# Optimization experiments

Hardware: AMD Instinct MI355X
Metric: run time of the kernel (lower is better)

## Reference

```python
import jax, jax.numpy as jnp
import numpy as np

COMMITMENT_COST = 0.25
NUM_CODES = 4096
EMBED_DIM = 64


def setup_inputs() -> dict:
    key = jax.random.key(0)
    k1, k2 = jax.random.split(key)
    z_e = jax.random.normal(k1, (65536, EMBED_DIM), dtype=jnp.float32)
    embeddings = jax.random.normal(k2, (NUM_CODES, EMBED_DIM), dtype=jnp.float32)
    return {"z_e": z_e, "embeddings": embeddings}


def reference(z_e, embeddings):
    # Squared Euclidean distances; argmin is identical to torch.cdist argmin.
    # d2[n,k] = |z_e[n]|^2 - 2 z_e[n].e[k] + |e[k]|^2
    z_sq = jnp.sum(z_e * z_e, axis=-1, keepdims=True)            # [N,1]
    e_sq = jnp.sum(embeddings * embeddings, axis=-1)              # [K]
    d2 = z_sq - 2.0 * jnp.einsum('nd,kd->nk', z_e, embeddings) + e_sq  # [N,K]
    indices = jnp.argmin(d2, axis=-1)                             # [N] int
    z_q = embeddings[indices]                                     # [N,D] gather

    # commitment loss = mse(stop_grad(z_q), z_e)
    commitment_loss = COMMITMENT_COST * jnp.mean(
        (jax.lax.stop_gradient(z_q) - z_e) ** 2)

    # straight-through estimator
    z_q_st = z_e + jax.lax.stop_gradient(z_q - z_e)

    # code usage stats: one-hot mean == normalized histogram (scatter-add)
    n = z_e.shape[0]
    counts = jnp.zeros((NUM_CODES,), dtype=jnp.float32).at[indices].add(1.0)
    avg_probs = counts / n
    perplexity = jnp.exp(-jnp.sum(avg_probs * jnp.log(avg_probs + 1e-10)))
    n_active = jnp.sum(avg_probs > 0.001)

    return z_q_st, indices, commitment_loss, perplexity, n_active
```

## Files before the change

kernel.cpp:

```cpp
#include <hip/hip_runtime.h>
#include <math.h>

#define D 64
#define K 4096
#define MARGIN 0.08f
#define KSPLIT 4
#define CPH (K / 16 / KSPLIT)

typedef float f32x4 __attribute__((ext_vector_type(4)));
typedef _Float16 f16x8 __attribute__((ext_vector_type(8)));

__global__ __launch_bounds__(256) void esplit_kernel(const float* __restrict__ emb,
                                                     short* __restrict__ e_h,
                                                     float* __restrict__ e_sq,
                                                     int* __restrict__ counts) {
  int i = blockIdx.x * 256 + threadIdx.x;
  {
    int lane = i & 63;
    int t = (i >> 6) & 1;
    int c = i >> 7;
    int quad = lane >> 4, col = lane & 15;
    const float* src = emb + (size_t)(c * 16 + col) * D + t * 32 + quad * 8;
    f32x4 u0 = *(const f32x4*)src;
    f32x4 u1 = *(const f32x4*)(src + 4);
    f16x8 h;
#pragma unroll
    for (int j = 0; j < 8; ++j) {
      float x = (j < 4) ? u0[j] : u1[j - 4];
      h[j] = (_Float16)x;
    }
    *(f16x8*)(e_h + (size_t)i * 8) = h;
  }
  if (i < K) {
    counts[i] = 0;
    const float* e = emb + (size_t)i * D;
    float s = 0.f;
#pragma unroll
    for (int d = 0; d < D; ++d) s = fmaf(e[d], e[d], s);
    e_sq[i] = s;
  }
}

__global__ __launch_bounds__(256, 2) void dist_kernel(const float* __restrict__ z_e,
                                                      const short* __restrict__ e_h,
                                                      const float* __restrict__ esq,
                                                      float* __restrict__ pbest,
                                                      float* __restrict__ psec,
                                                      int* __restrict__ pidx) {
  const int tid = threadIdx.x;
  const int wv = tid >> 6;
  const int lane = tid & 63;
  const int quad = lane >> 4, col = lane & 15;
  const int rowbase = blockIdx.x * 128 + wv * 32;
  const int half = blockIdx.y;
  const int c0 = half * CPH;

  f16x8 a_hi[2][2], a_lo[2][2];
#pragma unroll
  for (int s = 0; s < 2; ++s) {
#pragma unroll
    for (int t = 0; t < 2; ++t) {
      const float* zr = z_e + (size_t)(rowbase + s * 16 + col) * D + t * 32 + quad * 8;
      f32x4 u0 = *(const f32x4*)zr;
      f32x4 u1 = *(const f32x4*)(zr + 4);
#pragma unroll
      for (int j = 0; j < 8; ++j) {
        float x = (j < 4) ? u0[j] : u1[j - 4];
        _Float16 h = (_Float16)x;
        a_hi[s][t][j] = h;
        a_lo[s][t][j] = (_Float16)(x - (float)h);
      }
    }
  }

  float best[8], second[8];
  int bidx[8];
#pragma unroll
  for (int i = 0; i < 8; ++i) {
    best[i] = -__builtin_inff();
    second[i] = -__builtin_inff();
    bidx[i] = 0;
  }

  const size_t lofs = (size_t)lane * 8;
  const short* pB = e_h + (size_t)c0 * 1024 + lofs;
  const float* pE = esq + c0 * 16 + col;
  f16x8 b0 = *(const f16x8*)pB;
  f16x8 b1 = *(const f16x8*)(pB + 512);
  float eq = *pE;

  for (int cc = 0; cc < CPH; ++cc) {
    pB += 1024;
    pE += 16;
    f16x8 n0 = *(const f16x8*)pB;
    f16x8 n1 = *(const f16x8*)(pB + 512);
    float neq = *pE;

    const float seed = -0.5f * eq;
    f32x4 acc0 = {seed, seed, seed, seed};
    f32x4 acc1 = {seed, seed, seed, seed};
    acc0 = __builtin_amdgcn_mfma_f32_16x16x32_f16(a_hi[0][0], b0, acc0, 0, 0, 0);
    acc1 = __builtin_amdgcn_mfma_f32_16x16x32_f16(a_hi[1][0], b0, acc1, 0, 0, 0);
    acc0 = __builtin_amdgcn_mfma_f32_16x16x32_f16(a_lo[0][0], b0, acc0, 0, 0, 0);
    acc1 = __builtin_amdgcn_mfma_f32_16x16x32_f16(a_lo[1][0], b0, acc1, 0, 0, 0);
    acc0 = __builtin_amdgcn_mfma_f32_16x16x32_f16(a_hi[0][1], b1, acc0, 0, 0, 0);
    acc1 = __builtin_amdgcn_mfma_f32_16x16x32_f16(a_hi[1][1], b1, acc1, 0, 0, 0);
    acc0 = __builtin_amdgcn_mfma_f32_16x16x32_f16(a_lo[0][1], b1, acc0, 0, 0, 0);
    acc1 = __builtin_amdgcn_mfma_f32_16x16x32_f16(a_lo[1][1], b1, acc1, 0, 0, 0);

#pragma unroll
    for (int r = 0; r < 4; ++r) {
      float a0 = acc0[r];
      float ob = best[r];
      best[r] = fmaxf(ob, a0);
      second[r] = __builtin_amdgcn_fmed3f(ob, a0, second[r]);
      bidx[r] = (a0 > ob) ? cc : bidx[r];
    }
#pragma unroll
    for (int r = 0; r < 4; ++r) {
      float a1 = acc1[r];
      float ob = best[4 + r];
      best[4 + r] = fmaxf(ob, a1);
      second[4 + r] = __builtin_amdgcn_fmed3f(ob, a1, second[4 + r]);
      bidx[4 + r] = (a1 > ob) ? cc : bidx[4 + r];
    }

    b0 = n0;
    b1 = n1;
    eq = neq;
  }

#pragma unroll
  for (int i = 0; i < 8; ++i) {
    float b = -2.f * best[i];
    float s2 = -2.f * second[i];
    int ix = (c0 + bidx[i]) * 16 + col;
#pragma unroll
    for (int off = 1; off < 16; off <<= 1) {
      float ob = __shfl_xor(b, off);
      float os = __shfl_xor(s2, off);
      int oi = __shfl_xor(ix, off);
      float ns = fminf(fminf(s2, os), fmaxf(b, ob));
      if (ob < b || (ob == b && oi < ix)) ix = oi;
      b = fminf(b, ob);
      s2 = ns;
    }
    if (col == 0) {
      int row = rowbase + (i >> 2) * 16 + quad * 4 + (i & 3);
      size_t o = (size_t)half * 65536 + row;
      pbest[o] = b;
      psec[o] = s2;
      pidx[o] = ix;
    }
  }
}

__global__ __launch_bounds__(256) void merge_resolve_kernel(const float* __restrict__ z_e,
                                                            const float* __restrict__ emb,
                                                            const float* __restrict__ esq,
                                                            const float* __restrict__ pbest,
                                                            const float* __restrict__ psec,
                                                            const int* __restrict__ pidx,
                                                            int* __restrict__ best_idx) {
  const int tid = threadIdx.x;
  __shared__ int wl[256];
  __shared__ int wn;
  __shared__ float zs[4][D];
  if (tid == 0) wn = 0;
  __syncthreads();

  {
    int row = blockIdx.x * 256 + tid;
    float b = pbest[row];
    float s2 = psec[row];
    int ix = pidx[row];
#pragma unroll
    for (int h = 1; h < KSPLIT; ++h) {
      size_t o = (size_t)h * 65536 + row;
      float bh = pbest[o];
      float sh = psec[o];
      int ih = pidx[o];
      s2 = fminf(fminf(s2, sh), fmaxf(b, bh));
      if (bh < b) ix = ih;
      b = fminf(b, bh);
    }
    best_idx[row] = ix;
    if (s2 - b < MARGIN) {
      int slot = atomicAdd(&wn, 1);
      wl[slot] = row;
    }
  }
  __syncthreads();

  const int n = wn;
  const int wave = tid >> 6;
  const int lane = tid & 63;

  for (int j = wave; j < n; j += 4) {
    const int row = wl[j];
    if (lane < 16) ((f32x4*)zs[wave])[lane] = *((const f32x4*)(z_e + (size_t)row * D) + lane);

    float pb[KSPLIT], ps[KSPLIT];
    int pi[KSPLIT];
    float B = __builtin_inff();
#pragma unroll
    for (int h = 0; h < KSPLIT; ++h) {
      size_t o = (size_t)h * 65536 + row;
      pb[h] = pbest[o];
      ps[h] = psec[o];
      pi[h] = pidx[o];
      B = fminf(B, pb[h]);
    }
    const float lim = B + MARGIN;

    float bv = __builtin_inff();
    int bi = 0;
#pragma unroll
    for (int h = 0; h < KSPLIT; ++h) {
      if (ps[h] < lim) {
        float hb = __builtin_inff();
        int hx = 0;
        for (int t = 0; t < 16; ++t) {
          int c = h * 1024 + t * 64 + lane;
          const f32x4* er = (const f32x4*)(emb + (size_t)c * D);
          f32x4 a = {0.f, 0.f, 0.f, 0.f};
#pragma unroll
          for (int i = 0; i < 16; ++i)
            a = __builtin_elementwise_fma(er[i], ((const f32x4*)zs[wave])[i], a);
          float dot = (a[0] + a[1]) + (a[2] + a[3]);
          float q = fmaf(-2.f, dot, esq[c]);
          if (q < hb) { hb = q; hx = c; }
        }
#pragma unroll
        for (int off = 32; off > 0; off >>= 1) {
          float ov = __shfl_down(hb, off);
          int oi = __shfl_down(hx, off);
          if (ov < hb || (ov == hb && oi < hx)) { hb = ov; hx = oi; }
        }
        hb = __shfl(hb, 0);
        hx = __shfl(hx, 0);
        if (hb < bv || (hb == bv && hx < bi)) { bv = hb; bi = hx; }
      } else if (pb[h] < lim) {
        int c = pi[h];
        float p = emb[(size_t)c * D + lane] * zs[wave][lane];
#pragma unroll
        for (int off = 1; off < 64; off <<= 1) p += __shfl_xor(p, off);
        float q = fmaf(-2.f, p, esq[c]);
        if (q < bv || (q == bv && c < bi)) { bv = q; bi = c; }
      }
    }
    if (lane == 0) best_idx[row] = bi;
  }
}

__global__ __launch_bounds__(256) void finalize_kernel(const float* __restrict__ z_e,
                                                       const float* __restrict__ emb,
                                                       const int* __restrict__ best_idx,
                                                       float* __restrict__ out_zq,
                                                       float* __restrict__ out_idx,
                                                       int* __restrict__ counts,
                                                       float* __restrict__ block_loss) {
  const int tid = threadIdx.x;
  const int wave = tid >> 6;
  const int lane = tid & 63;
  const int row = blockIdx.x * 4 + wave;

  int bidx = best_idx[row];
  float ze = z_e[(size_t)row * D + lane];
  float zq = emb[(size_t)bidx * D + lane];
  float st = ze + (zq - ze);
  out_zq[(size_t)row * D + lane] = st;

  float diff = zq - ze;
  float sq = diff * diff;
#pragma unroll
  for (int off = 32; off > 0; off >>= 1) sq += __shfl_down(sq, off);

  __shared__ float ls[4];
  if (lane == 0) {
    ls[wave] = sq;
    out_idx[row] = (float)bidx;
    atomicAdd(&counts[bidx], 1);
  }
  __syncthreads();
  if (tid == 0) block_loss[blockIdx.x] = ls[0] + ls[1] + ls[2] + ls[3];
}

__global__ __launch_bounds__(1024) void stats_kernel(const float* __restrict__ block_loss,
                                                     int nblocks,
                                                     const int* __restrict__ counts,
                                                     float* __restrict__ out_scalars,
                                                     int N) {
  const int tid = threadIdx.x;
  const int wave = tid >> 6;
  const int lane = tid & 63;

  float lsum = 0.f;
  for (int i = tid; i < nblocks; i += 1024) lsum += block_loss[i];

  float ent = 0.f;
  int act = 0;
  const float invN = 1.0f / (float)N;
  for (int k = tid; k < K; k += 1024) {
    float p = (float)counts[k] * invN;
    ent += p * logf(p + 1e-10f);
    act += (p > 0.001f) ? 1 : 0;
  }

#pragma unroll
  for (int off = 32; off > 0; off >>= 1) {
    lsum += __shfl_down(lsum, off);
    ent += __shfl_down(ent, off);
    act += __shfl_down(act, off);
  }

  __shared__ float sl[16], se[16];
  __shared__ int sa[16];
  if (lane == 0) { sl[wave] = lsum; se[wave] = ent; sa[wave] = act; }
  __syncthreads();
  if (tid == 0) {
    float L = 0.f, E = 0.f;
    int A = 0;
#pragma unroll
    for (int w = 0; w < 16; ++w) { L += sl[w]; E += se[w]; A += sa[w]; }
    out_scalars[0] = 0.25f * L / ((float)N * (float)D);
    out_scalars[1] = expf(-E);
    out_scalars[2] = (float)A;
  }
}

extern "C" void kernel_launch(void* const* d_in, const int* in_sizes, int n_in,
                              void* d_out, int out_size, void* d_ws, size_t ws_size,
                              hipStream_t stream) {
  const float* z_e = (const float*)d_in[0];
  const float* emb = (const float*)d_in[1];
  const int N = in_sizes[0] / D;

  float* out = (float*)d_out;
  float* out_zq = out;
  float* out_idx = out + (size_t)N * D;
  float* out_scalars = out + (size_t)N * (D + 1);

  char* ws = (char*)d_ws;
  size_t o = 0;
  int* counts = (int*)(ws + o);      o += 16384;
  o += 256;
  float* esq = (float*)(ws + o);     o += 16384;
  short* e_h = (short*)(ws + o);     o += (size_t)K * D * 2;
  o += 8192;
  float* pbest = (float*)(ws + o);   o += (size_t)KSPLIT * N * 4;
  float* psec = (float*)(ws + o);    o += (size_t)KSPLIT * N * 4;
  int* pidx = (int*)(ws + o);        o += (size_t)KSPLIT * N * 4;
  int* best_idx = (int*)(ws + o);    o += (size_t)N * 4;
  float* block_loss = (float*)(ws + o);

  esplit_kernel<<<(K / 16) * 2 * 64 / 256, 256, 0, stream>>>(emb, e_h, esq, counts);
  dist_kernel<<<dim3(N / 128, KSPLIT), 256, 0, stream>>>(z_e, e_h, esq,
                                                         pbest, psec, pidx);
  merge_resolve_kernel<<<N / 256, 256, 0, stream>>>(z_e, emb, esq, pbest, psec,
                                                    pidx, best_idx);
  finalize_kernel<<<N / 4, 256, 0, stream>>>(z_e, emb, best_idx, out_zq, out_idx,
                                             counts, block_loss);
  stats_kernel<<<1, 1024, 0, stream>>>(block_loss, N / 4, counts, out_scalars, N);
}
```

Baseline: 224.9 us.

## Fuse merge, finalize and stats into one tail kernel; unroll distance loop

Merges the merge/resolve, finalize and stats kernels into a single tail kernel. It keeps the per-row best indices in shared memory, accumulates the loss into 64 atomic slots, and uses a last-block-done counter so the final block computes the scalar statistics. This removes two kernel launches and the global round trips for best_idx and block_loss. Separately, the dist_kernel main loop is unrolled by two with register ping-pong for the prefetched B fragments, which removes the register copies. The fused kernel processes 128 rows per block and relies on threadfence and atomics for cross-block completion, so that single final block becomes a serial tail.

```diff
diff --git a/kernel.cpp b/kernel.cpp
--- a/kernel.cpp
+++ b/kernel.cpp
@@ -13,7 +13,8 @@
 __global__ __launch_bounds__(256) void esplit_kernel(const float* __restrict__ emb,
                                                      short* __restrict__ e_h,
                                                      float* __restrict__ e_sq,
-                                                     int* __restrict__ counts) {
+                                                     int* __restrict__ counts,
+                                                     int* __restrict__ ctrl) {
   int i = blockIdx.x * 256 + threadIdx.x;
   {
     int lane = i & 63;
@@ -31,6 +32,7 @@
     }
     *(f16x8*)(e_h + (size_t)i * 8) = h;
   }
+  if (i < 128) ctrl[i] = 0;
   if (i < K) {
     counts[i] = 0;
     const float* e = emb + (size_t)i * D;
@@ -40,6 +42,45 @@
     e_sq[i] = s;
   }
 }
+
+#define MFMA16(A, B, C) __builtin_amdgcn_mfma_f32_16x16x32_f16(A, B, C, 0, 0, 0)
+
+#define STEP(C0, C1, CEQ, N0, N1, NEQ, CC)                                   \
+  {                                                                          \
+    N0 = *(const f16x8*)(pB);                                                \
+    N1 = *(const f16x8*)(pB + 512);                                          \
+    NEQ = *pE;                                                               \
+    pB += 1024;                                                              \
+    pE += 16;                                                                \
+    const float seed = -0.5f * (CEQ);                                        \
+    f32x4 acc0 = {seed, seed, seed, seed};                                   \
+    f32x4 acc1 = {seed, seed, seed, seed};                                   \
+    acc0 = MFMA16(a_hi[0][0], C0, acc0);                                     \
+    acc1 = MFMA16(a_hi[1][0], C0, acc1);                                     \
+    acc0 = MFMA16(a_lo[0][0], C0, acc0);                                     \
+    acc1 = MFMA16(a_lo[1][0], C0, acc1);                                     \
+    acc0 = MFMA16(a_hi[0][1], C1, acc0);                                     \
+    acc1 = MFMA16(a_hi[1][1], C1, acc1);                                     \
+    acc0 = MFMA16(a_lo[0][1], C1, acc0);                                     \
+    acc1 = MFMA16(a_lo[1][1], C1, acc1);                                     \
+    const int cc_ = (CC);                                                    \
+    _Pragma("unroll")                                                        \
+    for (int r = 0; r < 4; ++r) {                                            \
+      float a0 = acc0[r];                                                    \
+      float ob = best[r];                                                    \
+      best[r] = fmaxf(ob, a0);                                               \
+      second[r] = __builtin_amdgcn_fmed3f(ob, a0, second[r]);                \
+      bidx[r] = (a0 > ob) ? cc_ : bidx[r];                                   \
+    }                                                                        \
+    _Pragma("unroll")                                                        \
+    for (int r = 0; r < 4; ++r) {                                            \
+      float a1 = acc1[r];                                                    \
+      float ob = best[4 + r];                                                \
+      best[4 + r] = fmaxf(ob, a1);                                           \
+      second[4 + r] = __builtin_amdgcn_fmed3f(ob, a1, second[4 + r]);        \
+      bidx[4 + r] = (a1 > ob) ? cc_ : bidx[4 + r];                           \
+    }                                                                        \
+  }
 
 __global__ __launch_bounds__(256, 2) void dist_kernel(const float* __restrict__ z_e,
                                                       const short* __restrict__ e_h,
@@ -82,52 +123,19 @@
     bidx[i] = 0;
   }
 
-  const size_t lofs = (size_t)lane * 8;
-  const short* pB = e_h + (size_t)c0 * 1024 + lofs;
+  const short* pB = e_h + (size_t)c0 * 1024 + (size_t)lane * 8;
   const float* pE = esq + c0 * 16 + col;
   f16x8 b0 = *(const f16x8*)pB;
   f16x8 b1 = *(const f16x8*)(pB + 512);
   float eq = *pE;
-
-  for (int cc = 0; cc < CPH; ++cc) {
-    pB += 1024;
-    pE += 16;
-    f16x8 n0 = *(const f16x8*)pB;
-    f16x8 n1 = *(const f16x8*)(pB + 512);
-    float neq = *pE;
-
-    const float seed = -0.5f * eq;
-    f32x4 acc0 = {seed, seed, seed, seed};
-    f32x4 acc1 = {seed, seed, seed, seed};
-    acc0 = __builtin_amdgcn_mfma_f32_16x16x32_f16(a_hi[0][0], b0, acc0, 0, 0, 0);
-    acc1 = __builtin_amdgcn_mfma_f32_16x16x32_f16(a_hi[1][0], b0, acc1, 0, 0, 0);
-    acc0 = __builtin_amdgcn_mfma_f32_16x16x32_f16(a_lo[0][0], b0, acc0, 0, 0, 0);
-    acc1 = __builtin_amdgcn_mfma_f32_16x16x32_f16(a_lo[1][0], b0, acc1, 0, 0, 0);
-    acc0 = __builtin_amdgcn_mfma_f32_16x16x32_f16(a_hi[0][1], b1, acc0, 0, 0, 0);
-    acc1 = __builtin_amdgcn_mfma_f32_16x16x32_f16(a_hi[1][1], b1, acc1, 0, 0, 0);
-    acc0 = __builtin_amdgcn_mfma_f32_16x16x32_f16(a_lo[0][1], b1, acc0, 0, 0, 0);
-    acc1 = __builtin_amdgcn_mfma_f32_16x16x32_f16(a_lo[1][1], b1, acc1, 0, 0, 0);
-
-#pragma unroll
-    for (int r = 0; r < 4; ++r) {
-      float a0 = acc0[r];
-      float ob = best[r];
-      best[r] = fmaxf(ob, a0);
-      second[r] = __builtin_amdgcn_fmed3f(ob, a0, second[r]);
-      bidx[r] = (a0 > ob) ? cc : bidx[r];
-    }
-#pragma unroll
-    for (int r = 0; r < 4; ++r) {
-      float a1 = acc1[r];
-      float ob = best[4 + r];
-      best[4 + r] = fmaxf(ob, a1);
-      second[4 + r] = __builtin_amdgcn_fmed3f(ob, a1, second[4 + r]);
-      bidx[4 + r] = (a1 > ob) ? cc : bidx[4 + r];
-    }
-
-    b0 = n0;
-    b1 = n1;
-    eq = neq;
+  pB += 1024;
+  pE += 16;
+  f16x8 n0, n1;
+  float neq;
+
+  for (int cc = 0; cc < CPH; cc += 2) {
+    STEP(b0, b1, eq, n0, n1, neq, cc)
+    STEP(n0, n1, neq, b0, b1, eq, cc + 1)
   }
 
 #pragma unroll
@@ -155,22 +163,38 @@
   }
 }
 
-__global__ __launch_bounds__(256) void merge_resolve_kernel(const float* __restrict__ z_e,
-                                                            const float* __restrict__ emb,
-                                                            const float* __restrict__ esq,
-                                                            const float* __restrict__ pbest,
-                                                            const float* __restrict__ psec,
-                                                            const int* __restrict__ pidx,
-                                                            int* __restrict__ best_idx) {
+__global__ __launch_bounds__(256) void tail_kernel(const float* __restrict__ z_e,
+                                                   const float* __restrict__ emb,
+                                                   const float* __restrict__ esq,
+                                                   const float* __restrict__ pbest,
+                                                   const float* __restrict__ psec,
+                                                   const int* __restrict__ pidx,
+                                                   float* __restrict__ out_zq,
+                                                   float* __restrict__ out_idx,
+                                                   int* __restrict__ counts,
+                                                   int* __restrict__ ctrl,
+                                                   float* __restrict__ out_scalars,
+                                                   int N) {
   const int tid = threadIdx.x;
-  __shared__ int wl[256];
+  const int wave = tid >> 6;
+  const int lane = tid & 63;
+  const int base = blockIdx.x * 128;
+  int* done = ctrl;
+  float* loss_slots = (float*)(ctrl + 8);
+
+  __shared__ int wl[128];
+  __shared__ int bidx_s[128];
   __shared__ int wn;
+  __shared__ int lastflag;
   __shared__ float zs[4][D];
+  __shared__ float se[4];
+  __shared__ int sa[4];
+
   if (tid == 0) wn = 0;
   __syncthreads();
 
-  {
-    int row = blockIdx.x * 256 + tid;
+  if (tid < 128) {
+    int row = base + tid;
     float b = pbest[row];
     float s2 = psec[row];
     int ix = pidx[row];
@@ -184,7 +208,7 @@
       if (bh < b) ix = ih;
       b = fminf(b, bh);
     }
-    best_idx[row] = ix;
+    bidx_s[tid] = ix;
     if (s2 - b < MARGIN) {
       int slot = atomicAdd(&wn, 1);
       wl[slot] = row;
@@ -193,9 +217,6 @@
   __syncthreads();
 
   const int n = wn;
-  const int wave = tid >> 6;
-  const int lane = tid & 63;
-
   for (int j = wave; j < n; j += 4) {
     const int row = wl[j];
     if (lane < 16) ((f32x4*)zs[wave])[lane] = *((const f32x4*)(z_e + (size_t)row * D) + lane);
@@ -249,80 +270,69 @@
         if (q < bv || (q == bv && c < bi)) { bv = q; bi = c; }
       }
     }
-    if (lane == 0) best_idx[row] = bi;
-  }
-}
-
-__global__ __launch_bounds__(256) void finalize_kernel(const float* __restrict__ z_e,
-                                                       const float* __restrict__ emb,
-                                                       const int* __restrict__ best_idx,
-                                                       float* __restrict__ out_zq,
-                                                       float* __restrict__ out_idx,
-                                                       int* __restrict__ counts,
-                                                       float* __restrict__ block_loss) {
-  const int tid = threadIdx.x;
-  const int wave = tid >> 6;
-  const int lane = tid & 63;
-  const int row = blockIdx.x * 4 + wave;
-
-  int bidx = best_idx[row];
-  float ze = z_e[(size_t)row * D + lane];
-  float zq = emb[(size_t)bidx * D + lane];
-  float st = ze + (zq - ze);
-  out_zq[(size_t)row * D + lane] = st;
-
-  float diff = zq - ze;
-  float sq = diff * diff;
-#pragma unroll
-  for (int off = 32; off > 0; off >>= 1) sq += __shfl_down(sq, off);
-
-  __shared__ float ls[4];
-  if (lane == 0) {
-    ls[wave] = sq;
-    out_idx[row] = (float)bidx;
-    atomicAdd(&counts[bidx], 1);
-  }
-  __syncthreads();
-  if (tid == 0) block_loss[blockIdx.x] = ls[0] + ls[1] + ls[2] + ls[3];
-}
-
-__global__ __launch_bounds__(1024) void stats_kernel(const float* __restrict__ block_loss,
-                                                     int nblocks,
-                                                     const int* __restrict__ counts,
-                                                     float* __restrict__ out_scalars,
-                                                     int N) {
-  const int tid = threadIdx.x;
-  const int wave = tid >> 6;
-  const int lane = tid & 63;
-
-  float lsum = 0.f;
-  for (int i = tid; i < nblocks; i += 1024) lsum += block_loss[i];
+    if (lane == 0) bidx_s[row - base] = bi;
+  }
+  __syncthreads();
+
+  float lloss = 0.f;
+  for (int r = wave; r < 128; r += 8) {
+    const int r1 = r + 4;
+    const int i0 = bidx_s[r];
+    const int i1 = bidx_s[r1];
+    const size_t row0 = base + r, row1 = base + r1;
+    float ze0 = z_e[row0 * D + lane];
+    float ze1 = z_e[row1 * D + lane];
+    float zq0 = emb[(size_t)i0 * D + lane];
+    float zq1 = emb[(size_t)i1 * D + lane];
+    out_zq[row0 * D + lane] = ze0 + (zq0 - ze0);
+    out_zq[row1 * D + lane] = ze1 + (zq1 - ze1);
+    float d0 = zq0 - ze0, d1 = zq1 - ze1;
+    lloss = fmaf(d0, d0, lloss);
+    lloss = fmaf(d1, d1, lloss);
+    if (lane == 0) {
+      out_idx[row0] = (float)i0;
+      out_idx[row1] = (float)i1;
+      atomicAdd(&counts[i0], 1);
+      atomicAdd(&counts[i1], 1);
+    }
+  }
+#pragma unroll
+  for (int off = 32; off > 0; off >>= 1) lloss += __shfl_down(lloss, off);
+  if (lane == 0) atomicAdd(&loss_slots[blockIdx.x & 63], lloss);
+
+  __syncthreads();
+  if (tid == 0) {
+    __threadfence();
+    lastflag = (atomicAdd(done, 1) == (int)gridDim.x - 1);
+  }
+  __syncthreads();
+  if (!lastflag) return;
 
   float ent = 0.f;
   int act = 0;
   const float invN = 1.0f / (float)N;
-  for (int k = tid; k < K; k += 1024) {
-    float p = (float)counts[k] * invN;
+  for (int k = tid; k < K; k += 256) {
+    float p = (float)atomicAdd(&counts[k], 0) * invN;
     ent += p * logf(p + 1e-10f);
     act += (p > 0.001f) ? 1 : 0;
   }
-
 #pragma unroll
   for (int off = 32; off > 0; off >>= 1) {
-    lsum += __shfl_down(lsum, off);
     ent += __shfl_down(ent, off);
     act += __shfl_down(act, off);
   }
-
-  __shared__ float sl[16], se[16];
-  __shared__ int sa[16];
-  if (lane == 0) { sl[wave] = lsum; se[wave] = ent; sa[wave] = act; }
+  if (lane == 0) { se[wave] = ent; sa[wave] = act; }
+
+  float L = 0.f;
+  if (wave == 0) {
+    L = atomicAdd(&loss_slots[lane], 0.f);
+#pragma unroll
+    for (int off = 32; off > 0; off >>= 1) L += __shfl_down(L, off);
+  }
   __syncthreads();
   if (tid == 0) {
-    float L = 0.f, E = 0.f;
-    int A = 0;
-#pragma unroll
-    for (int w = 0; w < 16; ++w) { L += sl[w]; E += se[w]; A += sa[w]; }
+    float E = se[0] + se[1] + se[2] + se[3];
+    int A = sa[0] + sa[1] + sa[2] + sa[3];
     out_scalars[0] = 0.25f * L / ((float)N * (float)D);
     out_scalars[1] = expf(-E);
     out_scalars[2] = (float)A;
@@ -344,22 +354,19 @@
   char* ws = (char*)d_ws;
   size_t o = 0;
   int* counts = (int*)(ws + o);      o += 16384;
-  o += 256;
+  int* ctrl = (int*)(ws + o);        o += 512;
   float* esq = (float*)(ws + o);     o += 16384;
   short* e_h = (short*)(ws + o);     o += (size_t)K * D * 2;
   o += 8192;
   float* pbest = (float*)(ws + o);   o += (size_t)KSPLIT * N * 4;
   float* psec = (float*)(ws + o);    o += (size_t)KSPLIT * N * 4;
   int* pidx = (int*)(ws + o);        o += (size_t)KSPLIT * N * 4;
-  int* best_idx = (int*)(ws + o);    o += (size_t)N * 4;
-  float* block_loss = (float*)(ws + o);
-
-  esplit_kernel<<<(K / 16) * 2 * 64 / 256, 256, 0, stream>>>(emb, e_h, esq, counts);
+
+  esplit_kernel<<<(K / 16) * 2 * 64 / 256, 256, 0, stream>>>(emb, e_h, esq,
+                                                             counts, ctrl);
   dist_kernel<<<dim3(N / 128, KSPLIT), 256, 0, stream>>>(z_e, e_h, esq,
                                                          pbest, psec, pidx);
-  merge_resolve_kernel<<<N / 256, 256, 0, stream>>>(z_e, emb, esq, pbest, psec,
-                                                    pidx, best_idx);
-  finalize_kernel<<<N / 4, 256, 0, stream>>>(z_e, emb, best_idx, out_zq, out_idx,
-                                             counts, block_loss);
-  stats_kernel<<<1, 1024, 0, stream>>>(block_loss, N / 4, counts, out_scalars, N);
+  tail_kernel<<<N / 128, 256, 0, stream>>>(z_e, emb, esq, pbest, psec, pidx,
+                                           out_zq, out_idx, counts, ctrl,
+                                           out_scalars, N);
 }
```

After: 235.6 us. +4.8%, slower.
